# Performance work log

Measured on AMD Instinct MI355X. Metric: run time of the kernel, lower is better.

## Reference

```python
import jax, jax.numpy as jnp
import numpy as np

B, T, D_IN, D_OUT, H = 2, 2048, 1024, 1024, 16
HD = D_OUT // H


def setup_inputs() -> dict:
    key = jax.random.key(0)
    ks = jax.random.split(key, 6)
    s_in = 1.0 / np.sqrt(D_IN)
    s_out = 1.0 / np.sqrt(D_OUT)
    return {
        "x": jax.random.normal(ks[0], (B, T, D_IN), dtype=jnp.float32),
        # torch nn.Linear stores weight as (out_features, in_features)
        "Wq": jax.random.uniform(ks[1], (D_OUT, D_IN), jnp.float32, -s_in, s_in),
        "Wk": jax.random.uniform(ks[2], (D_OUT, D_IN), jnp.float32, -s_in, s_in),
        "Wv": jax.random.uniform(ks[3], (D_OUT, D_IN), jnp.float32, -s_in, s_in),
        "Wo": jax.random.uniform(ks[4], (D_OUT, D_OUT), jnp.float32, -s_out, s_out),
        "bo": jax.random.uniform(ks[5], (D_OUT,), jnp.float32, -s_out, s_out),
    }


def reference(x, Wq, Wk, Wv, Wo, bo):
    b, t, _ = x.shape
    q = jnp.einsum("btd,ed->bte", x, Wq).reshape(b, t, H, HD).transpose(0, 2, 1, 3)
    k = jnp.einsum("btd,ed->bte", x, Wk).reshape(b, t, H, HD).transpose(0, 2, 1, 3)
    v = jnp.einsum("btd,ed->bte", x, Wv).reshape(b, t, H, HD).transpose(0, 2, 1, 3)
    # [b, h, q, k] materialized scores, masked then scaled (as in source)
    scores = jnp.einsum("bhqd,bhkd->bhqk", q, k)
    causal = jnp.triu(jnp.ones((t, t), dtype=bool), k=1)
    scores = jnp.where(causal, -jnp.inf, scores)
    attn = jax.nn.softmax(scores / jnp.sqrt(jnp.float32(HD)), axis=-1)
    ctx = jnp.einsum("bhqk,bhkd->bhqd", attn, v)
    # NOTE: the source does .view(b, t, d_out) WITHOUT transposing (b,h,t,hd)
    # back to (b,t,h,hd). We replicate that reshape faithfully.
    ctx = ctx.reshape(b, t, D_OUT)
    return jnp.einsum("btd,ed->bte", ctx, Wo) + bo
```

## Files before the change

### kernel.cpp

```cpp
#include <hip/hip_runtime.h>
#include <math.h>

#define BB 2
#define TT 2048
#define DD 1024
#define NH 16
#define HDD 64

typedef __attribute__((ext_vector_type(8))) short v8s;
typedef __attribute__((ext_vector_type(4))) short v4s;
typedef __attribute__((ext_vector_type(4))) float f32x4;

__device__ __forceinline__ unsigned short f2bf(float f) {
    union { float f; unsigned int u; } c; c.f = f;
    unsigned int r = c.u + 0x7FFF + ((c.u >> 16) & 1);
    return (unsigned short)(r >> 16);
}

__device__ __forceinline__ v4s pack_bf16x4(float a, float b, float c, float d) {
#if __has_builtin(__builtin_amdgcn_cvt_pk_bf16_f32)
    auto lo = __builtin_amdgcn_cvt_pk_bf16_f32(a, b);
    auto hi = __builtin_amdgcn_cvt_pk_bf16_f32(c, d);
    union { v4s v; struct { decltype(lo) l; decltype(hi) h; } p; } u;
    u.p.l = lo; u.p.h = hi;
    return u.v;
#else
    v4s r;
    r[0] = (short)f2bf(a); r[1] = (short)f2bf(b);
    r[2] = (short)f2bf(c); r[3] = (short)f2bf(d);
    return r;
#endif
}

__device__ __forceinline__ float fexp2(float x) {
#if __has_builtin(__builtin_amdgcn_exp2f)
    return __builtin_amdgcn_exp2f(x);
#else
    float r; asm("v_exp_f32 %0, %1" : "=v"(r) : "v"(x)); return r;
#endif
}

__device__ __forceinline__ void gload_lds16(const void* g, void* l) {
    __builtin_amdgcn_global_load_lds(
        (const __attribute__((address_space(1))) void*)g,
        (__attribute__((address_space(3))) void*)l, 16, 0, 0);
}

__device__ __forceinline__ f32x4 mfma16x16x16bf16(v4s a, v4s b, f32x4 c) {
#if __has_builtin(__builtin_amdgcn_mfma_f32_16x16x16bf16_1k)
    return __builtin_amdgcn_mfma_f32_16x16x16bf16_1k(a, b, c, 0, 0, 0);
#else
    f32x4 d;
    asm("v_mfma_f32_16x16x16_bf16 %0, %1, %2, %0"
        : "=v"(d) : "v"(a), "v"(b), "0"(c));
    return d;
#endif
}

__global__ __launch_bounds__(256) void cast5_kernel(
    const float* __restrict__ x, const float* __restrict__ wq,
    const float* __restrict__ wk, const float* __restrict__ wv,
    const float* __restrict__ wo,
    unsigned short* __restrict__ xo, unsigned short* __restrict__ wqo,
    unsigned short* __restrict__ wko, unsigned short* __restrict__ wvo,
    unsigned short* __restrict__ woo)
{
    const float* s; unsigned short* d; int n4;
    switch (blockIdx.y) {
        case 0: s = x;  d = xo;  n4 = BB * TT * DD / 4; break;
        case 1: s = wq; d = wqo; n4 = DD * DD / 4; break;
        case 2: s = wk; d = wko; n4 = DD * DD / 4; break;
        case 3: s = wv; d = wvo; n4 = DD * DD / 4; break;
        default: s = wo; d = woo; n4 = DD * DD / 4; break;
    }
    int i = blockIdx.x * 256 + threadIdx.x;
    if (i < n4) {
        float4 v = ((const float4*)s)[i];
        ushort4 o;
        o.x = f2bf(v.x); o.y = f2bf(v.y); o.z = f2bf(v.z); o.w = f2bf(v.w);
        ((ushort4*)d)[i] = o;
    }
}

__global__ __launch_bounds__(256) void qkv_mfma(
    const unsigned short* __restrict__ x,
    const unsigned short* __restrict__ wq, const unsigned short* __restrict__ wk,
    const unsigned short* __restrict__ wv,
    unsigned short* __restrict__ qo, unsigned short* __restrict__ ko,
    unsigned short* __restrict__ vo)
{
    __shared__ unsigned short SMEM[16384];

    const int tid = threadIdx.x;
    const int lane = tid & 63;
    const int wid = tid >> 6;
    const int l15 = lane & 15, quad = lane >> 4;

    const int m0 = blockIdx.x << 7;
    const int ny = blockIdx.y;
    const int which = ny >> 3;
    const int n0 = (ny & 7) << 7;
    const unsigned short* W = (which == 0) ? wq : (which == 1) ? wk : wv;

    const int wm = (wid >> 1) << 6;
    const int wn = (wid & 1) << 6;

    const int f0 = (wid << 11) + (lane << 4);
    const int row0 = f0 >> 6, cs0 = (f0 & 63) >> 1;
    const int f1 = f0 + 1024;
    const int row1 = f1 >> 6, cs1 = (f1 & 63) >> 1;
    const int sw = (row0 & 3) << 3;
    const int csw0 = cs0 ^ sw, csw1 = cs1 ^ sw;
    const int rcol = ((quad ^ (l15 & 3)) << 4);

    char* const smem = (char*)SMEM;

#define QKV_STAGE(k0, buf)                                                     \
    do {                                                                       \
        gload_lds16(&x[(size_t)(m0 + row0) * DD + (k0) + csw0],                \
                    smem + (buf) * 8192 + f0);                                 \
        gload_lds16(&x[(size_t)(m0 + row1) * DD + (k0) + csw1],                \
                    smem + (buf) * 8192 + f1);                                 \
        gload_lds16(&W[(size_t)(n0 + row0) * DD + (k0) + csw0],                \
                    smem + 16384 + (buf) * 8192 + f0);                         \
        gload_lds16(&W[(size_t)(n0 + row1) * DD + (k0) + csw1],                \
                    smem + 16384 + (buf) * 8192 + f1);                         \
    } while (0)

    f32x4 acc[4][4] = {};

    QKV_STAGE(0, 0);
    __syncthreads();

    int cur = 0;
    for (int k0 = 0; k0 < DD; k0 += 32) {
        if (k0 + 32 < DD) QKV_STAGE(k0 + 32, cur ^ 1);

        const char* Ab = smem + cur * 8192;
        const char* Bb = smem + 16384 + cur * 8192;
        v8s af[4], bf[4];
#pragma unroll
        for (int i = 0; i < 4; ++i)
            af[i] = *(const v8s*)(Ab + (wm + (i << 4) + l15) * 64 + rcol);
#pragma unroll
        for (int j = 0; j < 4; ++j)
            bf[j] = *(const v8s*)(Bb + (wn + (j << 4) + l15) * 64 + rcol);
#pragma unroll
        for (int i = 0; i < 4; ++i)
#pragma unroll
            for (int j = 0; j < 4; ++j)
                acc[i][j] = __builtin_amdgcn_mfma_f32_16x16x32_bf16(af[i], bf[j], acc[i][j], 0, 0, 0);

        __syncthreads();
        cur ^= 1;
    }
#undef QKV_STAGE

    if (which == 2) {
#pragma unroll
        for (int i = 0; i < 4; ++i)
#pragma unroll
            for (int j = 0; j < 4; ++j) {
                const int n = n0 + wn + (j << 4) + l15;
                const int h = n >> 6, hd = n & 63;
                const int mb = m0 + wm + (i << 4) + (quad << 2);
                const int b = mb >> 11, t = mb & 2047;
                ushort4 pk;
                pk.x = f2bf(acc[i][j][0]); pk.y = f2bf(acc[i][j][1]);
                pk.z = f2bf(acc[i][j][2]); pk.w = f2bf(acc[i][j][3]);
                *(ushort4*)&vo[((((size_t)(b * NH + h) << 6) + hd) << 11) + t] = pk;
            }
    } else {
        unsigned short* outp = (which == 0) ? qo : ko;
        const float sc = (which == 1) ? 0.18033688011112042f : 1.0f;
#pragma unroll
        for (int p = 0; p < 2; ++p) {
            __syncthreads();
            if ((wid >> 1) == p) {
#pragma unroll
                for (int i = 0; i < 4; ++i)
#pragma unroll
                    for (int j = 0; j < 4; ++j)
#pragma unroll
                        for (int r = 0; r < 4; ++r) {
                            const int row = (i << 4) + (quad << 2) + r;
                            SMEM[row * 136 + wn + (j << 4) + l15] = f2bf(acc[i][j][r] * sc);
                        }
            }
            __syncthreads();
            const int rr = tid >> 2;
            const int cg = (tid & 3) << 5;
            const int m = m0 + (p << 6) + rr;
            const int b = m >> 11, t = m & 2047;
#pragma unroll
            for (int k2 = 0; k2 < 4; ++k2) {
                const int n = n0 + cg + (k2 << 3);
                const int h = n >> 6, hd = n & 63;
                const uint4 val = *(const uint4*)&SMEM[rr * 136 + cg + (k2 << 3)];
                *(uint4*)&outp[(((size_t)(b * NH + h) * TT + t) << 6) + hd] = val;
            }
        }
    }
}

__global__ __launch_bounds__(256) void attn_mfma(
    const unsigned short* __restrict__ q, const unsigned short* __restrict__ k,
    const unsigned short* __restrict__ vt, unsigned short* __restrict__ ctx)
{
    __shared__ unsigned short Ks[2][64][72];
    __shared__ unsigned short Vts[2][64][72];

    const int tid = threadIdx.x;
    const int lane = tid & 63;
    const int wid = tid >> 6;
    const int l15 = lane & 15, quad = lane >> 4;

    const int bh = blockIdx.x;
    const int qt = 31 - (int)blockIdx.y;
    const int q0 = qt << 6;
    const int qrow = q0 + (wid << 4) + l15;

    const unsigned short* qb = q + (size_t)bh * TT * HDD;
    const unsigned short* kb = k + (size_t)bh * TT * HDD;
    const unsigned short* vb = vt + (size_t)bh * HDD * TT;
    unsigned short* cb = ctx + (size_t)bh * TT * HDD;

    const int cr = tid >> 3;
    const int cc = (tid & 7) << 3;
    const int vsw = (cr & 8) << 2;
    const int ccv = cc ^ vsw;
    const int rsw = (l15 & 8) << 2;

    {
        uint4 k0r = *(const uint4*)&kb[(size_t)cr * HDD + cc];
        uint4 k1r = *(const uint4*)&kb[(size_t)(cr + 32) * HDD + cc];
        uint4 v0r = *(const uint4*)&vb[((size_t)cr << 11) + cc];
        uint4 v1r = *(const uint4*)&vb[((size_t)(cr + 32) << 11) + cc];
        *(uint4*)&Ks[0][cr][cc] = k0r;
        *(uint4*)&Ks[0][cr + 32][cc] = k1r;
        *(uint4*)&Vts[0][cr][ccv] = v0r;
        *(uint4*)&Vts[0][cr + 32][ccv] = v1r;
    }

    v8s qf[2];
#pragma unroll
    for (int c = 0; c < 2; ++c)
        qf[c] = *(const v8s*)&qb[(size_t)(q0 + (wid << 4) + l15) * HDD
                                 + (c << 5) + (quad << 3)];

    __syncthreads();

    float m_i = -INFINITY, l_i = 0.f;
    f32x4 o[4] = {};

    for (int jt = 0; jt <= qt; ++jt) {
        const int cur = jt & 1;

        uint4 k0r, k1r, v0r, v1r;
        const bool pre = (jt < qt);
        if (pre) {
            const int kn = (jt + 1) << 6;
            k0r = *(const uint4*)&kb[(size_t)(kn + cr) * HDD + cc];
            k1r = *(const uint4*)&kb[(size_t)(kn + cr + 32) * HDD + cc];
            v0r = *(const uint4*)&vb[((size_t)cr << 11) + kn + cc];
            v1r = *(const uint4*)&vb[((size_t)(cr + 32) << 11) + kn + cc];
        }

        const int k0 = jt << 6;

        f32x4 s[4] = {};
#pragma unroll
        for (int m = 0; m < 4; ++m) {
            const v8s kf0 = *(const v8s*)&Ks[cur][(m << 4) + l15][quad << 3];
            const v8s kf1 = *(const v8s*)&Ks[cur][(m << 4) + l15][32 + (quad << 3)];
            s[m] = __builtin_amdgcn_mfma_f32_16x16x32_bf16(kf0, qf[0], s[m], 0, 0, 0);
            s[m] = __builtin_amdgcn_mfma_f32_16x16x32_bf16(kf1, qf[1], s[m], 0, 0, 0);
        }

        if (jt == qt) {
#pragma unroll
            for (int m = 0; m < 4; ++m) {
                const int kc = k0 + (m << 4) + (quad << 2);
#pragma unroll
                for (int r = 0; r < 4; ++r)
                    if (kc + r > qrow) s[m][r] = -INFINITY;
            }
        }

        float mx = fmaxf(fmaxf(s[0][0], s[0][1]), fmaxf(s[0][2], s[0][3]));
        mx = fmaxf(mx, fmaxf(fmaxf(s[1][0], s[1][1]), fmaxf(s[1][2], s[1][3])));
        mx = fmaxf(mx, fmaxf(fmaxf(s[2][0], s[2][1]), fmaxf(s[2][2], s[2][3])));
        mx = fmaxf(mx, fmaxf(fmaxf(s[3][0], s[3][1]), fmaxf(s[3][2], s[3][3])));
        mx = fmaxf(mx, __shfl_xor(mx, 16));
        mx = fmaxf(mx, __shfl_xor(mx, 32));

        if (!__all(mx <= m_i + 8.0f)) {
            const float m_new = fmaxf(m_i, mx);
            const float alpha = fexp2(m_i - m_new);
            m_i = m_new;
            l_i *= alpha;
#pragma unroll
            for (int m = 0; m < 4; ++m)
#pragma unroll
                for (int r = 0; r < 4; ++r)
                    o[m][r] *= alpha;
        }

        float sum = 0.f;
        v4s pf[4];
#pragma unroll
        for (int m = 0; m < 4; ++m) {
            const float p0 = fexp2(s[m][0] - m_i);
            const float p1 = fexp2(s[m][1] - m_i);
            const float p2 = fexp2(s[m][2] - m_i);
            const float p3 = fexp2(s[m][3] - m_i);
            sum += (p0 + p1) + (p2 + p3);
            pf[m] = pack_bf16x4(p0, p1, p2, p3);
        }
        sum += __shfl_xor(sum, 16);
        sum += __shfl_xor(sum, 32);
        l_i += sum;

#pragma unroll
        for (int m = 0; m < 4; ++m)
#pragma unroll
            for (int c = 0; c < 4; ++c) {
                const v4s vf = *(const v4s*)&Vts[cur][(m << 4) + l15]
                                                    [(((c << 4) + (quad << 2)) ^ rsw)];
                o[m] = mfma16x16x16bf16(vf, pf[c], o[m]);
            }

        if (pre) {
            const int nxt = cur ^ 1;
            *(uint4*)&Ks[nxt][cr][cc] = k0r;
            *(uint4*)&Ks[nxt][cr + 32][cc] = k1r;
            *(uint4*)&Vts[nxt][cr][ccv] = v0r;
            *(uint4*)&Vts[nxt][cr + 32][ccv] = v1r;
        }
        __syncthreads();
    }

    const float linv = 1.f / l_i;
#pragma unroll
    for (int m = 0; m < 4; ++m) {
        ushort4 st;
        st.x = f2bf(o[m][0] * linv); st.y = f2bf(o[m][1] * linv);
        st.z = f2bf(o[m][2] * linv); st.w = f2bf(o[m][3] * linv);
        *(ushort4*)&cb[((size_t)qrow << 6) + (m << 4) + (quad << 2)] = st;
    }
}

__global__ __launch_bounds__(256) void oproj_mfma(
    const unsigned short* __restrict__ c, const unsigned short* __restrict__ wo,
    const float* __restrict__ bo, float* __restrict__ out)
{
    __shared__ unsigned short SMEM[16384];

    const int tid = threadIdx.x;
    const int lane = tid & 63;
    const int wid = tid >> 6;
    const int l15 = lane & 15, quad = lane >> 4;

    const int m0 = blockIdx.x << 7;
    const int n0 = blockIdx.y << 7;
    const int wm = (wid >> 1) << 6, wn = (wid & 1) << 6;

    const int f0 = (wid << 11) + (lane << 4);
    const int row0 = f0 >> 6, cs0 = (f0 & 63) >> 1;
    const int f1 = f0 + 1024;
    const int row1 = f1 >> 6, cs1 = (f1 & 63) >> 1;
    const int sw = (row0 & 3) << 3;
    const int csw0 = cs0 ^ sw, csw1 = cs1 ^ sw;
    const int rcol = ((quad ^ (l15 & 3)) << 4);

    char* const smem = (char*)SMEM;

#define OP_STAGE(k0, buf)                                                      \
    do {                                                                       \
        gload_lds16(&c[(size_t)(m0 + row0) * DD + (k0) + csw0],                \
                    smem + (buf) * 8192 + f0);                                 \
        gload_lds16(&c[(size_t)(m0 + row1) * DD + (k0) + csw1],                \
                    smem + (buf) * 8192 + f1);                                 \
        gload_lds16(&wo[(size_t)(n0 + row0) * DD + (k0) + csw0],               \
                    smem + 16384 + (buf) * 8192 + f0);                         \
        gload_lds16(&wo[(size_t)(n0 + row1) * DD + (k0) + csw1],               \
                    smem + 16384 + (buf) * 8192 + f1);                         \
    } while (0)

    f32x4 acc[4][4] = {};

    OP_STAGE(0, 0);
    __syncthreads();

    int cur = 0;
    for (int k0 = 0; k0 < DD; k0 += 32) {
        if (k0 + 32 < DD) OP_STAGE(k0 + 32, cur ^ 1);

        const char* Ab = smem + cur * 8192;
        const char* Bb = smem + 16384 + cur * 8192;
        v8s af[4], bf[4];
#pragma unroll
        for (int i = 0; i < 4; ++i)
            af[i] = *(const v8s*)(Ab + (wm + (i << 4) + l15) * 64 + rcol);
#pragma unroll
        for (int j = 0; j < 4; ++j)
            bf[j] = *(const v8s*)(Bb + (wn + (j << 4) + l15) * 64 + rcol);
#pragma unroll
        for (int i = 0; i < 4; ++i)
#pragma unroll
            for (int j = 0; j < 4; ++j)
                acc[i][j] = __builtin_amdgcn_mfma_f32_16x16x32_bf16(af[i], bf[j], acc[i][j], 0, 0, 0);

        __syncthreads();
        cur ^= 1;
    }
#undef OP_STAGE

#pragma unroll
    for (int j = 0; j < 4; ++j) {
        const int n = n0 + wn + (j << 4) + l15;
        const float bias = bo[n];
#pragma unroll
        for (int i = 0; i < 4; ++i) {
            const int mb = m0 + wm + (i << 4) + (quad << 2);
#pragma unroll
            for (int r = 0; r < 4; ++r)
                out[(size_t)(mb + r) * DD + n] = acc[i][j][r] + bias;
        }
    }
}

extern "C" void kernel_launch(void* const* d_in, const int* in_sizes, int n_in,
                              void* d_out, int out_size, void* d_ws, size_t ws_size,
                              hipStream_t stream) {
    const float* x  = (const float*)d_in[0];
    const float* Wq = (const float*)d_in[1];
    const float* Wk = (const float*)d_in[2];
    const float* Wv = (const float*)d_in[3];
    const float* Wo = (const float*)d_in[4];
    const float* bo = (const float*)d_in[5];
    float* out = (float*)d_out;

    const size_t NX = (size_t)BB * TT * DD;
    const size_t NW = (size_t)DD * DD;

    unsigned short* xb  = (unsigned short*)d_ws;
    unsigned short* wqb = xb + NX;
    unsigned short* wkb = wqb + NW;
    unsigned short* wvb = wkb + NW;
    unsigned short* wob = wvb + NW;
    unsigned short* qb  = wob + NW;
    unsigned short* kb  = qb + NX;
    unsigned short* vtb = kb + NX;
    unsigned short* cbuf = vtb + NX;

    cast5_kernel<<<dim3(4096, 5), 256, 0, stream>>>(x, Wq, Wk, Wv, Wo,
                                                    xb, wqb, wkb, wvb, wob);
    qkv_mfma<<<dim3(32, 24), 256, 0, stream>>>(xb, wqb, wkb, wvb, qb, kb, vtb);
    attn_mfma<<<dim3(32, 32), 256, 0, stream>>>(qb, kb, vtb, cbuf);
    oproj_mfma<<<dim3(32, 8), 256, 0, stream>>>(cbuf, wob, bo, out);
}
```

Before: 188.8 us.

## Double attention query tile to 128 rows so each wave handles two query groups

The attention kernel now gives each block 128 query rows, with each wave processing two 16-row groups. Every K/V tile loaded into shared memory is therefore reused across twice as many queries, halving K/V global traffic and block count. The lazy rescale check (skipping the rescale when the max grows by under 8) is dropped in favor of always rescaling. Costs are higher register pressure, fewer blocks (512) and less parallelism, plus masking now runs over the last two key tiles.

```diff
diff --git a/kernel.cpp b/kernel.cpp
--- a/kernel.cpp
+++ b/kernel.cpp
@@ -216,9 +216,10 @@
     const int l15 = lane & 15, quad = lane >> 4;
 
     const int bh = blockIdx.x;
-    const int qt = 31 - (int)blockIdx.y;
-    const int q0 = qt << 6;
-    const int qrow = q0 + (wid << 4) + l15;
+    const int qt = 15 - (int)blockIdx.y;
+    const int q0 = qt << 7;
+    const int nkt = (qt + 1) << 1;
+    const int qrow0 = q0 + (wid << 5) + l15;
 
     const unsigned short* qb = q + (size_t)bh * TT * HDD;
     const unsigned short* kb = k + (size_t)bh * TT * HDD;
@@ -242,22 +243,25 @@
         *(uint4*)&Vts[0][cr + 32][ccv] = v1r;
     }
 
-    v8s qf[2];
-#pragma unroll
-    for (int c = 0; c < 2; ++c)
-        qf[c] = *(const v8s*)&qb[(size_t)(q0 + (wid << 4) + l15) * HDD
-                                 + (c << 5) + (quad << 3)];
+    v8s qf[2][2];
+#pragma unroll
+    for (int g = 0; g < 2; ++g)
+#pragma unroll
+        for (int c = 0; c < 2; ++c)
+            qf[g][c] = *(const v8s*)&qb[(size_t)(qrow0 + (g << 4)) * HDD
+                                        + (c << 5) + (quad << 3)];
 
     __syncthreads();
 
-    float m_i = -INFINITY, l_i = 0.f;
-    f32x4 o[4] = {};
-
-    for (int jt = 0; jt <= qt; ++jt) {
+    float m_i[2] = {-INFINITY, -INFINITY};
+    float l_i[2] = {0.f, 0.f};
+    f32x4 o[2][4] = {};
+
+    for (int jt = 0; jt < nkt; ++jt) {
         const int cur = jt & 1;
 
         uint4 k0r, k1r, v0r, v1r;
-        const bool pre = (jt < qt);
+        const bool pre = (jt + 1 < nkt);
         if (pre) {
             const int kn = (jt + 1) << 6;
             k0r = *(const uint4*)&kb[(size_t)(kn + cr) * HDD + cc];
@@ -268,58 +272,68 @@
 
         const int k0 = jt << 6;
 
-        f32x4 s[4] = {};
+        f32x4 s[2][4];
+#pragma unroll
+        for (int g = 0; g < 2; ++g)
+#pragma unroll
+            for (int m = 0; m < 4; ++m) s[g][m] = f32x4{0.f, 0.f, 0.f, 0.f};
 #pragma unroll
         for (int m = 0; m < 4; ++m) {
             const v8s kf0 = *(const v8s*)&Ks[cur][(m << 4) + l15][quad << 3];
             const v8s kf1 = *(const v8s*)&Ks[cur][(m << 4) + l15][32 + (quad << 3)];
-            s[m] = __builtin_amdgcn_mfma_f32_16x16x32_bf16(kf0, qf[0], s[m], 0, 0, 0);
-            s[m] = __builtin_amdgcn_mfma_f32_16x16x32_bf16(kf1, qf[1], s[m], 0, 0, 0);
-        }
-
-        if (jt == qt) {
+            s[0][m] = __builtin_amdgcn_mfma_f32_16x16x32_bf16(kf0, qf[0][0], s[0][m], 0, 0, 0);
+            s[0][m] = __builtin_amdgcn_mfma_f32_16x16x32_bf16(kf1, qf[0][1], s[0][m], 0, 0, 0);
+            s[1][m] = __builtin_amdgcn_mfma_f32_16x16x32_bf16(kf0, qf[1][0], s[1][m], 0, 0, 0);
+            s[1][m] = __builtin_amdgcn_mfma_f32_16x16x32_bf16(kf1, qf[1][1], s[1][m], 0, 0, 0);
+        }
+
+        if (jt >= nkt - 2) {
+#pragma unroll
+            for (int g = 0; g < 2; ++g) {
+                const int qr = qrow0 + (g << 4);
+#pragma unroll
+                for (int m = 0; m < 4; ++m) {
+                    const int kc = k0 + (m << 4) + (quad << 2);
+#pragma unroll
+                    for (int r = 0; r < 4; ++r)
+                        if (kc + r > qr) s[g][m][r] = -INFINITY;
+                }
+            }
+        }
+
+        v4s pf[2][4];
+#pragma unroll
+        for (int g = 0; g < 2; ++g) {
+            float mx = fmaxf(fmaxf(s[g][0][0], s[g][0][1]), fmaxf(s[g][0][2], s[g][0][3]));
+            mx = fmaxf(mx, fmaxf(fmaxf(s[g][1][0], s[g][1][1]), fmaxf(s[g][1][2], s[g][1][3])));
+            mx = fmaxf(mx, fmaxf(fmaxf(s[g][2][0], s[g][2][1]), fmaxf(s[g][2][2], s[g][2][3])));
+            mx = fmaxf(mx, fmaxf(fmaxf(s[g][3][0], s[g][3][1]), fmaxf(s[g][3][2], s[g][3][3])));
+            mx = fmaxf(mx, __shfl_xor(mx, 16));
+            mx = fmaxf(mx, __shfl_xor(mx, 32));
+            const float m_new = fmaxf(m_i[g], mx);
+            const float alpha = fexp2(m_i[g] - m_new);
+            m_i[g] = m_new;
+
+            float sum = 0.f;
 #pragma unroll
             for (int m = 0; m < 4; ++m) {
-                const int kc = k0 + (m << 4) + (quad << 2);
+                const float p0 = fexp2(s[g][m][0] - m_new);
+                const float p1 = fexp2(s[g][m][1] - m_new);
+                const float p2 = fexp2(s[g][m][2] - m_new);
+                const float p3 = fexp2(s[g][m][3] - m_new);
+                sum += (p0 + p1) + (p2 + p3);
+                pf[g][m] = pack_bf16x4(p0, p1, p2, p3);
+            }
+            sum += __shfl_xor(sum, 16);
+            sum += __shfl_xor(sum, 32);
+            l_i[g] = l_i[g] * alpha + sum;
+
+#pragma unroll
+            for (int m = 0; m < 4; ++m)
 #pragma unroll
                 for (int r = 0; r < 4; ++r)
-                    if (kc + r > qrow) s[m][r] = -INFINITY;
-            }
-        }
-
-        float mx = fmaxf(fmaxf(s[0][0], s[0][1]), fmaxf(s[0][2], s[0][3]));
-        mx = fmaxf(mx, fmaxf(fmaxf(s[1][0], s[1][1]), fmaxf(s[1][2], s[1][3])));
-        mx = fmaxf(mx, fmaxf(fmaxf(s[2][0], s[2][1]), fmaxf(s[2][2], s[2][3])));
-        mx = fmaxf(mx, fmaxf(fmaxf(s[3][0], s[3][1]), fmaxf(s[3][2], s[3][3])));
-        mx = fmaxf(mx, __shfl_xor(mx, 16));
-        mx = fmaxf(mx, __shfl_xor(mx, 32));
-
-        if (!__all(mx <= m_i + 8.0f)) {
-            const float m_new = fmaxf(m_i, mx);
-            const float alpha = fexp2(m_i - m_new);
-            m_i = m_new;
-            l_i *= alpha;
-#pragma unroll
-            for (int m = 0; m < 4; ++m)
-#pragma unroll
-                for (int r = 0; r < 4; ++r)
-                    o[m][r] *= alpha;
-        }
-
-        float sum = 0.f;
-        v4s pf[4];
-#pragma unroll
-        for (int m = 0; m < 4; ++m) {
-            const float p0 = fexp2(s[m][0] - m_i);
-            const float p1 = fexp2(s[m][1] - m_i);
-            const float p2 = fexp2(s[m][2] - m_i);
-            const float p3 = fexp2(s[m][3] - m_i);
-            sum += (p0 + p1) + (p2 + p3);
-            pf[m] = pack_bf16x4(p0, p1, p2, p3);
-        }
-        sum += __shfl_xor(sum, 16);
-        sum += __shfl_xor(sum, 32);
-        l_i += sum;
+                    o[g][m][r] *= alpha;
+        }
 
 #pragma unroll
         for (int m = 0; m < 4; ++m)
@@ -327,7 +341,8 @@
             for (int c = 0; c < 4; ++c) {
                 const v4s vf = *(const v4s*)&Vts[cur][(m << 4) + l15]
                                                     [(((c << 4) + (quad << 2)) ^ rsw)];
-                o[m] = mfma16x16x16bf16(vf, pf[c], o[m]);
+                o[0][m] = mfma16x16x16bf16(vf, pf[0][c], o[0][m]);
+                o[1][m] = mfma16x16x16bf16(vf, pf[1][c], o[1][m]);
             }
 
         if (pre) {
@@ -340,13 +355,17 @@
         __syncthreads();
     }
 
-    const float linv = 1.f / l_i;
-#pragma unroll
-    for (int m = 0; m < 4; ++m) {
-        ushort4 st;
-        st.x = f2bf(o[m][0] * linv); st.y = f2bf(o[m][1] * linv);
-        st.z = f2bf(o[m][2] * linv); st.w = f2bf(o[m][3] * linv);
-        *(ushort4*)&cb[((size_t)qrow << 6) + (m << 4) + (quad << 2)] = st;
+#pragma unroll
+    for (int g = 0; g < 2; ++g) {
+        const float linv = 1.f / l_i[g];
+        const int qr = qrow0 + (g << 4);
+#pragma unroll
+        for (int m = 0; m < 4; ++m) {
+            ushort4 st;
+            st.x = f2bf(o[g][m][0] * linv); st.y = f2bf(o[g][m][1] * linv);
+            st.z = f2bf(o[g][m][2] * linv); st.w = f2bf(o[g][m][3] * linv);
+            *(ushort4*)&cb[((size_t)qr << 6) + (m << 4) + (quad << 2)] = st;
+        }
     }
 }
 
@@ -457,6 +476,6 @@
     cast5_kernel<<<dim3(4096, 5), 256, 0, stream>>>(x, Wq, Wk, Wv, Wo,
                                                     xb, wqb, wkb, wvb, wob);
     qkv_mfma<<<dim3(32, 24), 256, 0, stream>>>(xb, wqb, wkb, wvb, qb, kb, vtb);
-    attn_mfma<<<dim3(32, 32), 256, 0, stream>>>(qb, kb, vtb, cbuf);
+    attn_mfma<<<dim3(32, 16), 256, 0, stream>>>(qb, kb, vtb, cbuf);
     oproj_mfma<<<dim3(32, 8), 256, 0, stream>>>(cbuf, wob, bo, out);
 }
```

New measurement: 201.1 us. 6.5% more time.

## Use XOR-swizzled unpadded LDS tiles, stage Q through LDS, always rescale softmax

Applied to the files above, without the earlier changes.

The padded K/V shared tiles are replaced with unpadded 64x64 tiles that use an XOR swizzle on the row index to avoid bank conflicts. Q is now loaded coalesced into a swizzled LDS tile and read back as MFMA fragments, instead of each lane reading it directly from global memory. The conditional lazy rescale (skip when the max grows by less than 8) is replaced by an unconditional online-softmax rescale on every tile. This removes a wave-vote branch but adds multiplies on every iteration, and the extra Q buffer plus a barrier raise setup cost.

```diff
diff --git a/kernel.cpp b/kernel.cpp
--- a/kernel.cpp
+++ b/kernel.cpp
@@ -207,13 +207,15 @@
     const unsigned short* __restrict__ q, const unsigned short* __restrict__ k,
     const unsigned short* __restrict__ vt, unsigned short* __restrict__ ctx)
 {
-    __shared__ unsigned short Ks[2][64][72];
-    __shared__ unsigned short Vts[2][64][72];
+    __shared__ unsigned short Qs[64][64];
+    __shared__ unsigned short Ks[2][64][64];
+    __shared__ unsigned short Vts[2][64][64];
 
     const int tid = threadIdx.x;
     const int lane = tid & 63;
     const int wid = tid >> 6;
     const int l15 = lane & 15, quad = lane >> 4;
+    const int r7 = (l15 & 7) << 3;
 
     const int bh = blockIdx.x;
     const int qt = 31 - (int)blockIdx.y;
@@ -227,28 +229,30 @@
 
     const int cr = tid >> 3;
     const int cc = (tid & 7) << 3;
-    const int vsw = (cr & 8) << 2;
-    const int ccv = cc ^ vsw;
-    const int rsw = (l15 & 8) << 2;
-
+    const int cs = cc ^ ((cr & 7) << 3);
+
+#pragma unroll
+    for (int u = 0; u < 2; ++u) {
+        const int r = cr + (u << 5);
+        *(uint4*)&Qs[r][cs] = *(const uint4*)&qb[(size_t)(q0 + r) * HDD + cc];
+    }
     {
         uint4 k0r = *(const uint4*)&kb[(size_t)cr * HDD + cc];
         uint4 k1r = *(const uint4*)&kb[(size_t)(cr + 32) * HDD + cc];
         uint4 v0r = *(const uint4*)&vb[((size_t)cr << 11) + cc];
         uint4 v1r = *(const uint4*)&vb[((size_t)(cr + 32) << 11) + cc];
-        *(uint4*)&Ks[0][cr][cc] = k0r;
-        *(uint4*)&Ks[0][cr + 32][cc] = k1r;
-        *(uint4*)&Vts[0][cr][ccv] = v0r;
-        *(uint4*)&Vts[0][cr + 32][ccv] = v1r;
-    }
+        *(uint4*)&Ks[0][cr][cs] = k0r;
+        *(uint4*)&Ks[0][cr + 32][cs] = k1r;
+        *(uint4*)&Vts[0][cr][cs] = v0r;
+        *(uint4*)&Vts[0][cr + 32][cs] = v1r;
+    }
+    __syncthreads();
 
     v8s qf[2];
 #pragma unroll
     for (int c = 0; c < 2; ++c)
-        qf[c] = *(const v8s*)&qb[(size_t)(q0 + (wid << 4) + l15) * HDD
-                                 + (c << 5) + (quad << 3)];
-
-    __syncthreads();
+        qf[c] = *(const v8s*)&Qs[(wid << 4) + l15]
+                               [(((c << 5) + (quad << 3)) ^ r7)];
 
     float m_i = -INFINITY, l_i = 0.f;
     f32x4 o[4] = {};
@@ -269,10 +273,11 @@
         const int k0 = jt << 6;
 
         f32x4 s[4] = {};
+        const int kc0 = (quad << 3) ^ r7;
 #pragma unroll
         for (int m = 0; m < 4; ++m) {
-            const v8s kf0 = *(const v8s*)&Ks[cur][(m << 4) + l15][quad << 3];
-            const v8s kf1 = *(const v8s*)&Ks[cur][(m << 4) + l15][32 + (quad << 3)];
+            const v8s kf0 = *(const v8s*)&Ks[cur][(m << 4) + l15][kc0];
+            const v8s kf1 = *(const v8s*)&Ks[cur][(m << 4) + l15][kc0 ^ 32];
             s[m] = __builtin_amdgcn_mfma_f32_16x16x32_bf16(kf0, qf[0], s[m], 0, 0, 0);
             s[m] = __builtin_amdgcn_mfma_f32_16x16x32_bf16(kf1, qf[1], s[m], 0, 0, 0);
         }
@@ -293,49 +298,46 @@
         mx = fmaxf(mx, fmaxf(fmaxf(s[3][0], s[3][1]), fmaxf(s[3][2], s[3][3])));
         mx = fmaxf(mx, __shfl_xor(mx, 16));
         mx = fmaxf(mx, __shfl_xor(mx, 32));
-
-        if (!__all(mx <= m_i + 8.0f)) {
-            const float m_new = fmaxf(m_i, mx);
-            const float alpha = fexp2(m_i - m_new);
-            m_i = m_new;
-            l_i *= alpha;
-#pragma unroll
-            for (int m = 0; m < 4; ++m)
-#pragma unroll
-                for (int r = 0; r < 4; ++r)
-                    o[m][r] *= alpha;
-        }
+        const float m_new = fmaxf(m_i, mx);
+        const float alpha = fexp2(m_i - m_new);
+        m_i = m_new;
 
         float sum = 0.f;
         v4s pf[4];
 #pragma unroll
         for (int m = 0; m < 4; ++m) {
-            const float p0 = fexp2(s[m][0] - m_i);
-            const float p1 = fexp2(s[m][1] - m_i);
-            const float p2 = fexp2(s[m][2] - m_i);
-            const float p3 = fexp2(s[m][3] - m_i);
+            const float p0 = fexp2(s[m][0] - m_new);
+            const float p1 = fexp2(s[m][1] - m_new);
+            const float p2 = fexp2(s[m][2] - m_new);
+            const float p3 = fexp2(s[m][3] - m_new);
             sum += (p0 + p1) + (p2 + p3);
             pf[m] = pack_bf16x4(p0, p1, p2, p3);
         }
         sum += __shfl_xor(sum, 16);
         sum += __shfl_xor(sum, 32);
-        l_i += sum;
+        l_i = l_i * alpha + sum;
+
+#pragma unroll
+        for (int m = 0; m < 4; ++m)
+#pragma unroll
+            for (int r = 0; r < 4; ++r)
+                o[m][r] *= alpha;
 
 #pragma unroll
         for (int m = 0; m < 4; ++m)
 #pragma unroll
             for (int c = 0; c < 4; ++c) {
                 const v4s vf = *(const v4s*)&Vts[cur][(m << 4) + l15]
-                                                    [(((c << 4) + (quad << 2)) ^ rsw)];
+                                                    [(((c << 4) + (quad << 2)) ^ r7)];
                 o[m] = mfma16x16x16bf16(vf, pf[c], o[m]);
             }
 
         if (pre) {
             const int nxt = cur ^ 1;
-            *(uint4*)&Ks[nxt][cr][cc] = k0r;
-            *(uint4*)&Ks[nxt][cr + 32][cc] = k1r;
-            *(uint4*)&Vts[nxt][cr][ccv] = v0r;
-            *(uint4*)&Vts[nxt][cr + 32][ccv] = v1r;
+            *(uint4*)&Ks[nxt][cr][cs] = k0r;
+            *(uint4*)&Ks[nxt][cr + 32][cs] = k1r;
+            *(uint4*)&Vts[nxt][cr][cs] = v0r;
+            *(uint4*)&Vts[nxt][cr + 32][cs] = v1r;
         }
         __syncthreads();
     }
```

Result: faster. 182.3 us (-3.5%).
